# Kernel tuning notes

Hardware: AMD Instinct MI355X
Metric: run time of the kernel (lower is better)

The kernel has to match this reference:

```python
import jax, jax.numpy as jnp
import numpy as np

N_NODES = 100000
N_EDGES = 1600000
FEAT = 64
HIDDEN = 64
K_HOPS = 3
NUM_GRAPHS = 64
BN_EPS = 1e-5


def setup_inputs() -> dict:
    key = jax.random.key(0)
    k1, k2, k3, k4 = jax.random.split(key, 4)
    x = jax.random.normal(k1, (N_NODES, FEAT), dtype=jnp.float32)
    edge_index = jax.random.randint(k2, (2, N_EDGES), 0, N_NODES, dtype=jnp.int64)
    batch = jnp.sort(jax.random.randint(k3, (N_NODES,), 0, NUM_GRAPHS, dtype=jnp.int64))
    # Linear layer (xavier uniform, zero bias) of SGConv
    limit = float(np.sqrt(6.0 / (FEAT + HIDDEN)))
    W = jax.random.uniform(k4, (HIDDEN, FEAT), dtype=jnp.float32, minval=-limit, maxval=limit)
    b = jnp.zeros((HIDDEN,), dtype=jnp.float32)
    # BatchNorm1d affine params (fresh init: gamma=1, beta=0), training-mode stats
    gamma = jnp.ones((HIDDEN,), dtype=jnp.float32)
    beta = jnp.zeros((HIDDEN,), dtype=jnp.float32)
    return {"x": x, "edge_index": edge_index, "batch": batch,
            "W": W, "b": b, "gamma": gamma, "beta": beta}


def _sgc_forward(x, edge_index, batch, W, b, gamma, beta):
    N = x.shape[0]
    loop = jnp.arange(N, dtype=edge_index.dtype)
    src = jnp.concatenate([edge_index[0], loop])  # row (source)
    dst = jnp.concatenate([edge_index[1], loop])  # col (target)
    # gcn_norm: deg over target index with unit edge weights (incl. self loops)
    deg = jax.ops.segment_sum(jnp.ones_like(src, dtype=x.dtype), dst, num_segments=N)
    dinv = jnp.where(deg > 0, jax.lax.rsqrt(deg), 0.0)
    norm = (dinv[src] * dinv[dst])[:, None]  # [E+N, 1]
    # K hops of normalized propagation: h <- A_hat h
    h = x
    for _ in range(K_HOPS):
        h = jax.ops.segment_sum(h[src] * norm, dst, num_segments=N)
    # linear + relu
    h = jax.nn.relu(h @ W.T + b)
    # BatchNorm1d in training mode (biased variance over nodes)
    mean = jnp.mean(h, axis=0)
    var = jnp.mean(jnp.square(h - mean), axis=0)
    h = gamma * (h - mean) * jax.lax.rsqrt(var + BN_EPS) + beta
    # global_add_pool by graph id
    pooled = jax.ops.segment_sum(h, batch, num_segments=NUM_GRAPHS)
    return pooled, h


def reference(x, edge_index, batch, W, b, gamma, beta):
    return _sgc_forward(x, edge_index, batch, W, b, gamma, beta)
```

## Files before the change

### kernel.cpp

```cpp
#include <hip/hip_runtime.h>
#include <hip/hip_fp16.h>

#define NN 100000
#define NE 1600000
#define F 64
#define NG 64
#define BN_EPS 1e-5f
#define EPB 8192
#define NT ((NE + EPB - 1) / EPB)
#define NPB 128
#define NBKT ((NN + NPB - 1) / NPB)
#define M_CNT (NBKT * NT)
#define NSB ((M_CNT + 1023) / 1024)
#define CAP 3072
#define NLB ((NN + 63) / 64)
#define RED_B 16
#define RPB ((NLB + RED_B - 1) / RED_B)

typedef _Float16 half8 __attribute__((ext_vector_type(8)));
typedef float f32x4 __attribute__((ext_vector_type(4)));

__device__ __forceinline__ float fatomic_add(float* p, float v) {
    return unsafeAtomicAdd(p, v);
}

__global__ void k_init(float* __restrict__ pooled, float* __restrict__ sums,
                       const float* __restrict__ Wg, __half* __restrict__ Wh) {
    int i = blockIdx.x * blockDim.x + threadIdx.x;
    if (i < NG * F) pooled[i] = 0.f;
    if (i < 2 * F) sums[i] = 0.f;
    if (i < F * F) Wh[i] = __float2half(Wg[i]);
}

__global__ __launch_bounds__(256) void kA1(const int* __restrict__ dst,
                                           int* __restrict__ cnt) {
    __shared__ int hist[NBKT];
    int t = threadIdx.x;
    for (int i = t; i < NBKT; i += 256) hist[i] = 0;
    __syncthreads();
    int base = blockIdx.x * EPB;
#pragma unroll
    for (int r = 0; r < EPB / 256; ++r) {
        int e = base + r * 256 + t;
        if (e < NE) atomicAdd(&hist[dst[e] >> 7], 1);
    }
    __syncthreads();
    for (int i = t; i < NBKT; i += 256)
        cnt[i * NT + blockIdx.x] = hist[i];
}

__global__ __launch_bounds__(1024) void kS1(const int* __restrict__ cnt,
                                            int* __restrict__ part) {
    int t = threadIdx.x;
    int i = blockIdx.x * 1024 + t;
    int v = (i < M_CNT) ? cnt[i] : 0;
#pragma unroll
    for (int o = 32; o > 0; o >>= 1) v += __shfl_down(v, o, 64);
    __shared__ int ws[16];
    if ((t & 63) == 0) ws[t >> 6] = v;
    __syncthreads();
    if (t == 0) {
        int s = 0;
#pragma unroll
        for (int k = 0; k < 16; ++k) s += ws[k];
        part[blockIdx.x] = s;
    }
}

__global__ __launch_bounds__(256) void kS2(int* __restrict__ part) {
    __shared__ int sh[256];
    int t = threadIdx.x;
    int v = (t < NSB) ? part[t] : 0;
    sh[t] = v;
    __syncthreads();
    for (int o = 1; o < 256; o <<= 1) {
        int u = (t >= o) ? sh[t - o] : 0;
        __syncthreads();
        sh[t] += u;
        __syncthreads();
    }
    if (t < NSB) part[t] = sh[t] - v;
}

__global__ __launch_bounds__(1024) void kS3(const int* __restrict__ cnt,
                                            const int* __restrict__ part,
                                            int* __restrict__ cscan) {
    __shared__ int sh[1024];
    int t = threadIdx.x;
    int i = blockIdx.x * 1024 + t;
    int v = (i < M_CNT) ? cnt[i] : 0;
    sh[t] = v;
    __syncthreads();
    for (int o = 1; o < 1024; o <<= 1) {
        int u = (t >= o) ? sh[t - o] : 0;
        __syncthreads();
        sh[t] += u;
        __syncthreads();
    }
    if (i < M_CNT) cscan[i] = part[blockIdx.x] + sh[t] - v;
}

__global__ __launch_bounds__(256) void kA3(const int* __restrict__ src,
                                           const int* __restrict__ dst,
                                           const int* __restrict__ cscan,
                                           int2* __restrict__ pairs) {
    __shared__ int hoff[NBKT];
    int t = threadIdx.x;
    for (int i = t; i < NBKT; i += 256) hoff[i] = cscan[i * NT + blockIdx.x];
    __syncthreads();
    int base = blockIdx.x * EPB;
#pragma unroll
    for (int r = 0; r < EPB / 256; ++r) {
        int e = base + r * 256 + t;
        if (e < NE) {
            int d = dst[e], s = src[e];
            int pos = atomicAdd(&hoff[d >> 7], 1);
            pairs[pos] = make_int2(d, s);
        }
    }
}

__global__ __launch_bounds__(256) void kB2(const int2* __restrict__ pairs,
                                           const int* __restrict__ cscan,
                                           int* __restrict__ csrc,
                                           int* __restrict__ offs,
                                           float* __restrict__ dinv,
                                           float* __restrict__ dn2) {
    __shared__ int ld[CAP], ls[CAP], lo[CAP];
    __shared__ int hist[NPB], pre[NPB], curl[NPB];
    int b = blockIdx.x, t = threadIdx.x;
    int s = cscan[b * NT];
    int e = (b == NBKT - 1) ? NE : cscan[(b + 1) * NT];
    int cnt = min(e - s, CAP);
    int nbase = b * NPB;
    if (t < NPB) hist[t] = 0;
    __syncthreads();
    for (int i = t; i < cnt; i += 256) {
        int2 p = pairs[s + i];
        int dl = p.x - nbase;
        ld[i] = dl; ls[i] = p.y;
        atomicAdd(&hist[dl], 1);
    }
    __syncthreads();
    int dg = (t < NPB) ? hist[t] : 0;
    if (t < NPB) pre[t] = dg;
    __syncthreads();
    for (int o = 1; o < NPB; o <<= 1) {
        int u = (t < NPB && t >= o) ? pre[t - o] : 0;
        __syncthreads();
        if (t < NPB) pre[t] += u;
        __syncthreads();
    }
    if (t < NPB) {
        int ex = pre[t] - dg;
        curl[t] = ex;
        int n = nbase + t;
        if (n < NN) {
            offs[n] = s + ex;
            float r = rsqrtf((float)(dg + 1));
            dinv[n] = r;
            dn2[n] = r * r;
        }
    }
    if (b == 0 && t == 0) offs[NN] = NE;
    __syncthreads();
    for (int i = t; i < cnt; i += 256) {
        int pos = atomicAdd(&curl[ld[i]], 1);
        lo[pos] = ls[i];
    }
    __syncthreads();
    for (int i = t; i < cnt; i += 256) csrc[s + i] = lo[i];
}

__global__ void k_u0(const float2* __restrict__ x2, const float* __restrict__ dinv,
                     __half2* __restrict__ u2) {
    int i = blockIdx.x * blockDim.x + threadIdx.x;
    if (i >= NN * F / 2) return;
    float2 v = x2[i];
    float d = dinv[i >> 5];
    u2[i] = __floats2half2_rn(v.x * d, v.y * d);
}

__global__ __launch_bounds__(256) void k_hop(const int* __restrict__ offs,
                                             const int* __restrict__ csrc,
                                             const float* __restrict__ oscale,
                                             const __half2* __restrict__ uin,
                                             __half2* __restrict__ uout) {
    int wv = blockIdx.x * 4 + (threadIdx.x >> 6);
    int lane = threadIdx.x & 63;
    int n = wv * 2 + (lane >> 5);
    int c = lane & 31;
    float2 acc = __half22float2(uin[n * 32 + c]);
    int e = offs[n], end = offs[n + 1];
    for (; e + 8 <= end; e += 8) {
        int s0 = csrc[e],     s1 = csrc[e + 1], s2 = csrc[e + 2], s3 = csrc[e + 3];
        int s4 = csrc[e + 4], s5 = csrc[e + 5], s6 = csrc[e + 6], s7 = csrc[e + 7];
        float2 f0 = __half22float2(uin[s0 * 32 + c]);
        float2 f1 = __half22float2(uin[s1 * 32 + c]);
        float2 f2 = __half22float2(uin[s2 * 32 + c]);
        float2 f3 = __half22float2(uin[s3 * 32 + c]);
        float2 f4 = __half22float2(uin[s4 * 32 + c]);
        float2 f5 = __half22float2(uin[s5 * 32 + c]);
        float2 f6 = __half22float2(uin[s6 * 32 + c]);
        float2 f7 = __half22float2(uin[s7 * 32 + c]);
        acc.x += ((f0.x + f1.x) + (f2.x + f3.x)) + ((f4.x + f5.x) + (f6.x + f7.x));
        acc.y += ((f0.y + f1.y) + (f2.y + f3.y)) + ((f4.y + f5.y) + (f6.y + f7.y));
    }
    for (; e < end; ++e) {
        float2 f = __half22float2(uin[csrc[e] * 32 + c]);
        acc.x += f.x; acc.y += f.y;
    }
    float os = oscale[n];
    uout[n * 32 + c] = __floats2half2_rn(acc.x * os, acc.y * os);
}

__global__ __launch_bounds__(256) void k_linear(const __half* __restrict__ h,
                                                const __half* __restrict__ Wh,
                                                const float* __restrict__ bg,
                                                __half* __restrict__ y,
                                                float* __restrict__ psum) {
    __shared__ float sred[4][64], qred[4][64];
    int tid = threadIdx.x;
    int wid = tid >> 6, lane = tid & 63;
    int lo = lane & 15, hi = lane >> 4;
    int n0 = blockIdx.x * 64 + wid * 16;

    half8 bf[4][2];
#pragma unroll
    for (int ct = 0; ct < 4; ++ct)
#pragma unroll
        for (int kk = 0; kk < 2; ++kk)
            bf[ct][kk] = *(const half8*)(Wh + (ct * 16 + lo) * 64 + kk * 32 + hi * 8);

    int arow = n0 + lo;
    half8 af[2];
    if (arow < NN) {
        af[0] = *(const half8*)(h + arow * 64 + hi * 8);
        af[1] = *(const half8*)(h + arow * 64 + 32 + hi * 8);
    } else {
#pragma unroll
        for (int j = 0; j < 8; ++j) { af[0][j] = (_Float16)0; af[1][j] = (_Float16)0; }
    }

    f32x4 acc[4];
#pragma unroll
    for (int ct = 0; ct < 4; ++ct) {
        acc[ct] = (f32x4){0.f, 0.f, 0.f, 0.f};
        acc[ct] = __builtin_amdgcn_mfma_f32_16x16x32_f16(af[0], bf[ct][0], acc[ct], 0, 0, 0);
        acc[ct] = __builtin_amdgcn_mfma_f32_16x16x32_f16(af[1], bf[ct][1], acc[ct], 0, 0, 0);
    }

#pragma unroll
    for (int ct = 0; ct < 4; ++ct) {
        int j = ct * 16 + lo;
        float bj = bg[j];
        float ls = 0.f, lq = 0.f;
#pragma unroll
        for (int r = 0; r < 4; ++r) {
            int n = n0 + hi * 4 + r;
            if (n < NN) {
                float v = fmaxf(acc[ct][r] + bj, 0.f);
                y[n * 64 + j] = __float2half(v);
                ls += v; lq += v * v;
            }
        }
        ls += __shfl_xor(ls, 16, 64); ls += __shfl_xor(ls, 32, 64);
        lq += __shfl_xor(lq, 16, 64); lq += __shfl_xor(lq, 32, 64);
        if (hi == 0) { sred[wid][j] = ls; qred[wid][j] = lq; }
    }
    __syncthreads();
    if (tid < 128) {
        int c = tid & 63;
        float v = (tid < 64)
            ? (sred[0][c] + sred[1][c] + sred[2][c] + sred[3][c])
            : (qred[0][c] + qred[1][c] + qred[2][c] + qred[3][c]);
        psum[blockIdx.x * 128 + tid] = v;
    }
}

__global__ __launch_bounds__(256) void k_red(const float* __restrict__ psum,
                                             float* __restrict__ sums) {
    int t = threadIdx.x;
    int c = t & 127, half = t >> 7;
    int r0 = blockIdx.x * RPB + half;
    int r1 = min((int)(blockIdx.x + 1) * RPB, NLB);
    float s = 0.f;
    for (int r = r0; r < r1; r += 2)
        s += psum[r * 128 + c];
    __shared__ float sh[128];
    if (half == 0) sh[c] = s;
    __syncthreads();
    if (half == 1) {
        float v = s + sh[c];
        fatomic_add(&sums[c], v);
    }
}

__global__ __launch_bounds__(256) void k_normpool(const __half* __restrict__ y,
                                                  const int* __restrict__ batch,
                                                  const float* __restrict__ sums,
                                                  const float* __restrict__ gamma,
                                                  const float* __restrict__ beta,
                                                  float* __restrict__ outh,
                                                  float* __restrict__ pooled) {
    int tid = threadIdx.x;
    int j = tid & 63, nl = tid >> 6;
    float mean = sums[j] * (1.0f / NN);
    float var = sums[64 + j] * (1.0f / NN) - mean * mean;
    float rinv = rsqrtf(var + BN_EPS);
    float a = gamma[j] * rinv;
    float c = beta[j] - mean * a;
    int base = blockIdx.x * 256;
    int curg = -1;
    float acc = 0.f;
    for (int it = 0; it < 64; ++it) {
        int n = base + it * 4 + nl;
        if (n >= NN) break;
        int g = batch[n];
        float v = fmaf(__half2float(y[n * 64 + j]), a, c);
        outh[(size_t)n * 64 + j] = v;
        if (g != curg) {
            if (curg >= 0) fatomic_add(&pooled[curg * 64 + j], acc);
            curg = g; acc = 0.f;
        }
        acc += v;
    }
    if (curg >= 0) fatomic_add(&pooled[curg * 64 + j], acc);
}

extern "C" void kernel_launch(void* const* d_in, const int* in_sizes, int n_in,
                              void* d_out, int out_size, void* d_ws, size_t ws_size,
                              hipStream_t stream) {
    const float* x     = (const float*)d_in[0];
    const int*   ei    = (const int*)d_in[1];
    const int*   batch = (const int*)d_in[2];
    const float* W     = (const float*)d_in[3];
    const float* b     = (const float*)d_in[4];
    const float* gamma = (const float*)d_in[5];
    const float* beta  = (const float*)d_in[6];
    const int* src = ei;
    const int* dst = ei + NE;

    float* pooled = (float*)d_out;
    float* outh   = (float*)d_out + NG * F;

    char* w = (char*)d_ws;
    float* dinv  = (float*)w;  w += sizeof(float) * NN;
    float* dn2   = (float*)w;  w += sizeof(float) * NN;
    int*   offs  = (int*)w;    w += sizeof(int) * (NN + 1);
    float* sums  = (float*)w;  w += sizeof(float) * 2 * F;
    __half* Wh   = (__half*)w; w += sizeof(__half) * F * F;
    float* psum  = (float*)w;  w += sizeof(float) * NLB * 128;
    int*   cnt   = (int*)w;    w += sizeof(int) * M_CNT;
    int*   cscan = (int*)w;    w += sizeof(int) * M_CNT;
    int*   part  = (int*)w;    w += sizeof(int) * 256;
    int*   csrc  = (int*)w;    w += sizeof(int) * NE;
    char* uni = w;
    __half* ubufA = (__half*)uni;
    __half* ubufB = (__half*)(uni + sizeof(__half) * NN * F);
    int2*   pairs = (int2*)uni;

    const int B = 256;
    dim3 blk(B);

    k_init<<<dim3((NN + B - 1) / B), blk, 0, stream>>>(pooled, sums, W, Wh);
    kA1<<<dim3(NT), blk, 0, stream>>>(dst, cnt);
    kS1<<<dim3(NSB), dim3(1024), 0, stream>>>(cnt, part);
    kS2<<<dim3(1), blk, 0, stream>>>(part);
    kS3<<<dim3(NSB), dim3(1024), 0, stream>>>(cnt, part, cscan);
    kA3<<<dim3(NT), blk, 0, stream>>>(src, dst, cscan, pairs);
    kB2<<<dim3(NBKT), blk, 0, stream>>>(pairs, cscan, csrc, offs, dinv, dn2);

    k_u0<<<dim3((NN * F / 2 + B - 1) / B), blk, 0, stream>>>((const float2*)x, dinv, (__half2*)ubufA);

    dim3 gh(NN / 8);
    k_hop<<<gh, blk, 0, stream>>>(offs, csrc, dn2,  (const __half2*)ubufA, (__half2*)ubufB);
    k_hop<<<gh, blk, 0, stream>>>(offs, csrc, dn2,  (const __half2*)ubufB, (__half2*)ubufA);
    k_hop<<<gh, blk, 0, stream>>>(offs, csrc, dinv, (const __half2*)ubufA, (__half2*)ubufB);

    __half* yh = ubufA;
    k_linear<<<dim3(NLB), blk, 0, stream>>>(ubufB, Wh, b, yh, psum);
    k_red<<<dim3(RED_B), blk, 0, stream>>>(psum, sums);
    k_normpool<<<dim3((NN + 255) / 256), blk, 0, stream>>>(yh, batch, sums, gamma, beta, outh, pooled);
}
```

Baseline: 278.2 us.

## Replace global bucket scan with per-tile local sort and packed edge pairs

The CSR build no longer runs a global histogram, a three-kernel scan and a separate scatter pass. Each edge tile now stages its edges in shared memory, sorts them locally by destination bucket, writes per-tile bucket prefixes, and packs source and local destination into one int. A single-block kernel scans the bucket totals, and the bucket kernel gathers its segments from every tile. The init kernel is folded into the first kernel. This cuts launches and halves the pair traffic, but the gather in kB2 is a serial per-thread loop over the tile segments and kSB runs as one block looping over all tiles.

```diff
diff --git a/kernel.cpp b/kernel.cpp
--- a/kernel.cpp
+++ b/kernel.cpp
@@ -10,8 +10,6 @@
 #define NT ((NE + EPB - 1) / EPB)
 #define NPB 128
 #define NBKT ((NN + NPB - 1) / NPB)
-#define M_CNT (NBKT * NT)
-#define NSB ((M_CNT + 1023) / 1024)
 #define CAP 3072
 #define NLB ((NN + 63) / 64)
 #define RED_B 16
@@ -24,152 +22,172 @@
     return unsafeAtomicAdd(p, v);
 }
 
-__global__ void k_init(float* __restrict__ pooled, float* __restrict__ sums,
-                       const float* __restrict__ Wg, __half* __restrict__ Wh) {
-    int i = blockIdx.x * blockDim.x + threadIdx.x;
-    if (i < NG * F) pooled[i] = 0.f;
-    if (i < 2 * F) sums[i] = 0.f;
-    if (i < F * F) Wh[i] = __float2half(Wg[i]);
-}
-
-__global__ __launch_bounds__(256) void kA1(const int* __restrict__ dst,
-                                           int* __restrict__ cnt) {
-    __shared__ int hist[NBKT];
-    int t = threadIdx.x;
-    for (int i = t; i < NBKT; i += 256) hist[i] = 0;
-    __syncthreads();
-    int base = blockIdx.x * EPB;
+__global__ __launch_bounds__(256) void kA1(const int* __restrict__ src,
+                                           const int* __restrict__ dst,
+                                           int* __restrict__ pairs,
+                                           int* __restrict__ tpre,
+                                           float* __restrict__ pooled,
+                                           float* __restrict__ sums,
+                                           const float* __restrict__ Wg,
+                                           __half* __restrict__ Wh) {
+    __shared__ int stage[EPB];
+    __shared__ unsigned short keyv[EPB];
+    __shared__ int hist[1024];
+    __shared__ int curb[1024];
+    __shared__ int ps[256];
+    int t = blockIdx.x, tid = threadIdx.x;
+
+    int gi = t * 256 + tid;
+    if (gi < NG * F) pooled[gi] = 0.f;
+    if (gi < 2 * F) sums[gi] = 0.f;
+    if (gi < F * F) Wh[gi] = __float2half(Wg[gi]);
+
+    for (int i = tid; i < 1024; i += 256) hist[i] = 0;
+    __syncthreads();
+
+    int base = t * EPB;
+    int nE = min(EPB, NE - base);
 #pragma unroll
     for (int r = 0; r < EPB / 256; ++r) {
-        int e = base + r * 256 + t;
-        if (e < NE) atomicAdd(&hist[dst[e] >> 7], 1);
-    }
-    __syncthreads();
-    for (int i = t; i < NBKT; i += 256)
-        cnt[i * NT + blockIdx.x] = hist[i];
-}
-
-__global__ __launch_bounds__(1024) void kS1(const int* __restrict__ cnt,
-                                            int* __restrict__ part) {
-    int t = threadIdx.x;
-    int i = blockIdx.x * 1024 + t;
-    int v = (i < M_CNT) ? cnt[i] : 0;
-#pragma unroll
-    for (int o = 32; o > 0; o >>= 1) v += __shfl_down(v, o, 64);
-    __shared__ int ws[16];
-    if ((t & 63) == 0) ws[t >> 6] = v;
-    __syncthreads();
-    if (t == 0) {
-        int s = 0;
-#pragma unroll
-        for (int k = 0; k < 16; ++k) s += ws[k];
-        part[blockIdx.x] = s;
-    }
-}
-
-__global__ __launch_bounds__(256) void kS2(int* __restrict__ part) {
-    __shared__ int sh[256];
-    int t = threadIdx.x;
-    int v = (t < NSB) ? part[t] : 0;
-    sh[t] = v;
+        int i = r * 256 + tid;
+        if (i < nE) {
+            int d = dst[base + i], s = src[base + i];
+            int key = d >> 7;
+            keyv[i] = (unsigned short)key;
+            stage[i] = s | ((d & 127) << 17);
+            atomicAdd(&hist[key], 1);
+        }
+    }
+    __syncthreads();
+    int h0 = hist[4 * tid], h1 = hist[4 * tid + 1], h2 = hist[4 * tid + 2], h3 = hist[4 * tid + 3];
+    int lsum = h0 + h1 + h2 + h3;
+    ps[tid] = lsum;
     __syncthreads();
     for (int o = 1; o < 256; o <<= 1) {
-        int u = (t >= o) ? sh[t - o] : 0;
-        __syncthreads();
-        sh[t] += u;
-        __syncthreads();
-    }
-    if (t < NSB) part[t] = sh[t] - v;
-}
-
-__global__ __launch_bounds__(1024) void kS3(const int* __restrict__ cnt,
-                                            const int* __restrict__ part,
-                                            int* __restrict__ cscan) {
-    __shared__ int sh[1024];
-    int t = threadIdx.x;
-    int i = blockIdx.x * 1024 + t;
-    int v = (i < M_CNT) ? cnt[i] : 0;
-    sh[t] = v;
+        int u = (tid >= o) ? ps[tid - o] : 0;
+        __syncthreads();
+        ps[tid] += u;
+        __syncthreads();
+    }
+    int ex = ps[tid] - lsum;
+    int p0 = ex, p1 = ex + h0, p2 = p1 + h1, p3 = p2 + h2;
+    {
+        int bb = 4 * tid;
+        if (bb < NBKT)     { tpre[t * NBKT + bb]     = p0; curb[bb]     = p0; }
+        if (bb + 1 < NBKT) { tpre[t * NBKT + bb + 1] = p1; curb[bb + 1] = p1; }
+        if (bb + 2 < NBKT) { tpre[t * NBKT + bb + 2] = p2; curb[bb + 2] = p2; }
+        if (bb + 3 < NBKT) { tpre[t * NBKT + bb + 3] = p3; curb[bb + 3] = p3; }
+    }
+    __syncthreads();
+#pragma unroll
+    for (int r = 0; r < EPB / 256; ++r) {
+        int i = r * 256 + tid;
+        if (i < nE) {
+            int pos = atomicAdd(&curb[keyv[i]], 1);
+            pairs[base + pos] = stage[i];
+        }
+    }
+}
+
+__global__ __launch_bounds__(1024) void kSB(const int* __restrict__ tpre,
+                                            int* __restrict__ bstart) {
+    __shared__ int tot[1024];
+    int tid = threadIdx.x;
+    int acc = 0;
+    for (int t = 0; t < NT; ++t) {
+        if (tid < NBKT) {
+            int a = tpre[t * NBKT + tid];
+            int bnd = (tid == NBKT - 1) ? min(EPB, NE - t * EPB) : tpre[t * NBKT + tid + 1];
+            acc += bnd - a;
+        }
+    }
+    tot[tid] = (tid < NBKT) ? acc : 0;
     __syncthreads();
     for (int o = 1; o < 1024; o <<= 1) {
-        int u = (t >= o) ? sh[t - o] : 0;
-        __syncthreads();
-        sh[t] += u;
-        __syncthreads();
-    }
-    if (i < M_CNT) cscan[i] = part[blockIdx.x] + sh[t] - v;
-}
-
-__global__ __launch_bounds__(256) void kA3(const int* __restrict__ src,
-                                           const int* __restrict__ dst,
-                                           const int* __restrict__ cscan,
-                                           int2* __restrict__ pairs) {
-    __shared__ int hoff[NBKT];
-    int t = threadIdx.x;
-    for (int i = t; i < NBKT; i += 256) hoff[i] = cscan[i * NT + blockIdx.x];
-    __syncthreads();
-    int base = blockIdx.x * EPB;
-#pragma unroll
-    for (int r = 0; r < EPB / 256; ++r) {
-        int e = base + r * 256 + t;
-        if (e < NE) {
-            int d = dst[e], s = src[e];
-            int pos = atomicAdd(&hoff[d >> 7], 1);
-            pairs[pos] = make_int2(d, s);
-        }
-    }
-}
-
-__global__ __launch_bounds__(256) void kB2(const int2* __restrict__ pairs,
-                                           const int* __restrict__ cscan,
+        int u = (tid >= o) ? tot[tid - o] : 0;
+        __syncthreads();
+        tot[tid] += u;
+        __syncthreads();
+    }
+    if (tid < NBKT) bstart[tid] = tot[tid] - acc;
+    if (tid == NBKT - 1) bstart[NBKT] = tot[tid];
+}
+
+__global__ __launch_bounds__(256) void kB2(const int* __restrict__ pairs,
+                                           const int* __restrict__ tpre,
+                                           const int* __restrict__ bstart,
                                            int* __restrict__ csrc,
                                            int* __restrict__ offs,
                                            float* __restrict__ dinv,
                                            float* __restrict__ dn2) {
-    __shared__ int ld[CAP], ls[CAP], lo[CAP];
-    __shared__ int hist[NPB], pre[NPB], curl[NPB];
-    int b = blockIdx.x, t = threadIdx.x;
-    int s = cscan[b * NT];
-    int e = (b == NBKT - 1) ? NE : cscan[(b + 1) * NT];
-    int cnt = min(e - s, CAP);
-    int nbase = b * NPB;
-    if (t < NPB) hist[t] = 0;
-    __syncthreads();
-    for (int i = t; i < cnt; i += 256) {
-        int2 p = pairs[s + i];
-        int dl = p.x - nbase;
-        ld[i] = dl; ls[i] = p.y;
-        atomicAdd(&hist[dl], 1);
-    }
-    __syncthreads();
-    int dg = (t < NPB) ? hist[t] : 0;
-    if (t < NPB) pre[t] = dg;
+    __shared__ int lsrc[CAP];
+    __shared__ unsigned char ldl[CAP];
+    __shared__ int lo[CAP];
+    __shared__ int toff[NT], rstart[NT];
+    __shared__ int sc[256];
+    __shared__ int hist[NPB], pre2[NPB], curl[NPB];
+    int b = blockIdx.x, tid = threadIdx.x;
+    int s0 = bstart[b];
+
+    int len = 0;
+    if (tid < NT) {
+        int a = tpre[tid * NBKT + b];
+        int bnd = (b == NBKT - 1) ? min(EPB, NE - tid * EPB) : tpre[tid * NBKT + b + 1];
+        rstart[tid] = a;
+        len = bnd - a;
+    }
+    sc[tid] = len;
+    __syncthreads();
+    for (int o = 1; o < 256; o <<= 1) {
+        int u = (tid >= o) ? sc[tid - o] : 0;
+        __syncthreads();
+        sc[tid] += u;
+        __syncthreads();
+    }
+    if (tid < NT) toff[tid] = sc[tid] - len;
+    int cnt = min(sc[255], CAP);
+    __syncthreads();
+    if (tid < NT) {
+        int o2 = toff[tid];
+        const int* p = pairs + tid * EPB + rstart[tid];
+        for (int k = 0; k < len && o2 + k < CAP; ++k) {
+            int pk = p[k];
+            lsrc[o2 + k] = pk & 0x1FFFF;
+            ldl[o2 + k] = (unsigned char)(pk >> 17);
+        }
+    }
+    if (tid < NPB) hist[tid] = 0;
+    __syncthreads();
+    for (int i = tid; i < cnt; i += 256) atomicAdd(&hist[ldl[i]], 1);
+    __syncthreads();
+    int dg = (tid < NPB) ? hist[tid] : 0;
+    if (tid < NPB) pre2[tid] = dg;
     __syncthreads();
     for (int o = 1; o < NPB; o <<= 1) {
-        int u = (t < NPB && t >= o) ? pre[t - o] : 0;
-        __syncthreads();
-        if (t < NPB) pre[t] += u;
-        __syncthreads();
-    }
-    if (t < NPB) {
-        int ex = pre[t] - dg;
-        curl[t] = ex;
-        int n = nbase + t;
+        int u = (tid < NPB && tid >= o) ? pre2[tid - o] : 0;
+        __syncthreads();
+        if (tid < NPB) pre2[tid] += u;
+        __syncthreads();
+    }
+    if (tid < NPB) {
+        int exn = pre2[tid] - dg;
+        curl[tid] = exn;
+        int n = b * NPB + tid;
         if (n < NN) {
-            offs[n] = s + ex;
+            offs[n] = s0 + exn;
             float r = rsqrtf((float)(dg + 1));
             dinv[n] = r;
             dn2[n] = r * r;
         }
     }
-    if (b == 0 && t == 0) offs[NN] = NE;
-    __syncthreads();
-    for (int i = t; i < cnt; i += 256) {
-        int pos = atomicAdd(&curl[ld[i]], 1);
-        lo[pos] = ls[i];
-    }
-    __syncthreads();
-    for (int i = t; i < cnt; i += 256) csrc[s + i] = lo[i];
+    if (b == 0 && tid == 0) offs[NN] = NE;
+    __syncthreads();
+    for (int i = tid; i < cnt; i += 256) {
+        int pos = atomicAdd(&curl[ldl[i]], 1);
+        lo[pos] = lsrc[i];
+    }
+    __syncthreads();
+    for (int i = tid; i < cnt; i += 256) csrc[s0 + i] = lo[i];
 }
 
 __global__ void k_u0(const float2* __restrict__ x2, const float* __restrict__ dinv,
@@ -290,10 +308,7 @@
     __shared__ float sh[128];
     if (half == 0) sh[c] = s;
     __syncthreads();
-    if (half == 1) {
-        float v = s + sh[c];
-        fatomic_add(&sums[c], v);
-    }
+    if (half == 1) fatomic_add(&sums[c], s + sh[c]);
 }
 
 __global__ __launch_bounds__(256) void k_normpool(const __half* __restrict__ y,
@@ -345,31 +360,26 @@
     float* outh   = (float*)d_out + NG * F;
 
     char* w = (char*)d_ws;
-    float* dinv  = (float*)w;  w += sizeof(float) * NN;
-    float* dn2   = (float*)w;  w += sizeof(float) * NN;
-    int*   offs  = (int*)w;    w += sizeof(int) * (NN + 1);
-    float* sums  = (float*)w;  w += sizeof(float) * 2 * F;
-    __half* Wh   = (__half*)w; w += sizeof(__half) * F * F;
-    float* psum  = (float*)w;  w += sizeof(float) * NLB * 128;
-    int*   cnt   = (int*)w;    w += sizeof(int) * M_CNT;
-    int*   cscan = (int*)w;    w += sizeof(int) * M_CNT;
-    int*   part  = (int*)w;    w += sizeof(int) * 256;
-    int*   csrc  = (int*)w;    w += sizeof(int) * NE;
+    float* dinv   = (float*)w;  w += sizeof(float) * NN;
+    float* dn2    = (float*)w;  w += sizeof(float) * NN;
+    int*   offs   = (int*)w;    w += sizeof(int) * (NN + 1);
+    float* sums   = (float*)w;  w += sizeof(float) * 2 * F;
+    __half* Wh    = (__half*)w; w += sizeof(__half) * F * F;
+    float* psum   = (float*)w;  w += sizeof(float) * NLB * 128;
+    int*   tpre   = (int*)w;    w += sizeof(int) * NT * NBKT;
+    int*   bstart = (int*)w;    w += sizeof(int) * (NBKT + 1);
+    int*   csrc   = (int*)w;    w += sizeof(int) * NE;
     char* uni = w;
     __half* ubufA = (__half*)uni;
     __half* ubufB = (__half*)(uni + sizeof(__half) * NN * F);
-    int2*   pairs = (int2*)uni;
+    int*    pairs = (int*)uni;
 
     const int B = 256;
     dim3 blk(B);
 
-    k_init<<<dim3((NN + B - 1) / B), blk, 0, stream>>>(pooled, sums, W, Wh);
-    kA1<<<dim3(NT), blk, 0, stream>>>(dst, cnt);
-    kS1<<<dim3(NSB), dim3(1024), 0, stream>>>(cnt, part);
-    kS2<<<dim3(1), blk, 0, stream>>>(part);
-    kS3<<<dim3(NSB), dim3(1024), 0, stream>>>(cnt, part, cscan);
-    kA3<<<dim3(NT), blk, 0, stream>>>(src, dst, cscan, pairs);
-    kB2<<<dim3(NBKT), blk, 0, stream>>>(pairs, cscan, csrc, offs, dinv, dn2);
+    kA1<<<dim3(NT), blk, 0, stream>>>(src, dst, pairs, tpre, pooled, sums, W, Wh);
+    kSB<<<dim3(1), dim3(1024), 0, stream>>>(tpre, bstart);
+    kB2<<<dim3(NBKT), blk, 0, stream>>>(pairs, tpre, bstart, csrc, offs, dinv, dn2);
 
     k_u0<<<dim3((NN * F / 2 + B - 1) / B), blk, 0, stream>>>((const float2*)x, dinv, (__half2*)ubufA);
 
```

After: 325.9 us. 1.17x slower.
